# Optimization experiments

Hardware: AMD Instinct MI355X
Metric: run time of the kernel (lower is better)

## Reference

```python
import jax, jax.numpy as jnp
import numpy as np

E = 262144   # num edges
T = 1048576  # num triplets
H = 128      # hidden_channels
IE = 64      # int_emb_size
NR = 6       # num_radial
NS = 7       # num_spherical
BD = 8       # basis_emb_size_dist
BA = 8       # basis_emb_size_angle


def setup_inputs() -> dict:
    key = jax.random.key(0)
    ks = jax.random.split(key, 32)
    def rnd(k, shape, s=0.1):
        return jax.random.normal(k, shape, dtype=jnp.float32) * s
    return {
        "x1": rnd(ks[0], (T, H), 1.0),
        "x_old": rnd(ks[1], (E, H), 1.0),
        "rbf0": rnd(ks[2], (E, NR), 1.0),
        "sbf": rnd(ks[3], (T, NS * NR), 1.0),
        "idx_kj": jax.random.randint(ks[4], (T,), 0, E),
        "idx_ji": jax.random.randint(ks[5], (T,), 0, E),
        "W_rbf1": rnd(ks[6], (NR, BD)),
        "W_rbf2": rnd(ks[7], (BD, H)),
        "W_sbf1": rnd(ks[8], (NS * NR, BA)),
        "W_sbf2": rnd(ks[9], (BA, IE)),
        "W_rbf": rnd(ks[10], (NR, H)),
        "W_kj": rnd(ks[11], (H, H)), "b_kj": rnd(ks[12], (H,)),
        "W_ji": rnd(ks[13], (H, H)), "b_ji": rnd(ks[14], (H,)),
        "W_connect": rnd(ks[15], (H, H)), "b_connect": rnd(ks[16], (H,)),
        "W_get_up": rnd(ks[17], (H, H)), "b_get_up": rnd(ks[18], (H,)),
        "W_down": rnd(ks[19], (H, IE)), "b_down": rnd(ks[20], (IE,)),
        "W_up": rnd(ks[21], (IE, H)), "b_up": rnd(ks[22], (H,)),
        "res_before_W": rnd(ks[23], (1, 2, H, H)), "res_before_b": rnd(ks[24], (1, 2, H)),
        "W_lin": rnd(ks[25], (H, H)), "b_lin": rnd(ks[26], (H,)),
        "res_after_W": rnd(ks[27], (2, 2, H, H)), "res_after_b": rnd(ks[28], (2, 2, H)),
    }


def _residual(x, W, b):
    # x + act(lin2(act(lin1(x))))
    h = jax.nn.silu(x @ W[0] + b[0])
    return x + jax.nn.silu(h @ W[1] + b[1])


def reference(x1, x_old, rbf0, sbf, idx_kj, idx_ji, W_rbf1, W_rbf2, W_sbf1, W_sbf2,
              W_rbf, W_kj, b_kj, W_ji, b_ji, W_connect, b_connect, W_get_up, b_get_up,
              W_down, b_down, W_up, b_up, res_before_W, res_before_b, W_lin, b_lin,
              res_after_W, res_after_b):
    act = jax.nn.silu  # swish
    nE = x_old.shape[0]
    # aggregate plane features onto edges
    x_up = jax.ops.segment_sum(x1, idx_ji, num_segments=nE)
    x_up = act(x_up @ W_get_up + b_get_up)
    x_ji = act(x_old @ W_ji + b_ji)
    x_kj = act(x_old @ W_kj + b_kj)
    rbf = (rbf0 @ W_rbf1) @ W_rbf2            # [E, H]
    x_kj = x_kj * rbf
    x_kj = act(x_kj @ W_down + b_down)        # [E, IE]
    sbf_p = (sbf @ W_sbf1) @ W_sbf2           # [T, IE]
    x_kj = x_kj[idx_kj] * sbf_p               # gather edges -> triplets
    x_kj = jax.ops.segment_sum(x_kj, idx_ji, num_segments=nE)  # scatter back to edges
    x_kj = act(x_kj @ W_up + b_up)
    e1 = x_ji + x_kj
    e1 = act(e1 @ W_connect + b_connect) + x_up
    for i in range(res_before_W.shape[0]):
        e1 = _residual(e1, res_before_W[i], res_before_b[i])
    e1 = act(e1 @ W_lin + b_lin) + x_old
    for i in range(res_after_W.shape[0]):
        e1 = _residual(e1, res_after_W[i], res_after_b[i])
    e2 = (rbf0 @ W_rbf) * e1
    return (e1, e2)
```

## Files before the change

### kernel.cpp

```cpp
#include <hip/hip_runtime.h>

#define E_N 262144
#define T_N 1048576

typedef short  bf16x8  __attribute__((ext_vector_type(8)));
typedef float  f32x4   __attribute__((ext_vector_type(4)));

#define OFF_KJ    0
#define OFF_DOWN  16384
#define OFF_UP    24576
#define OFF_JI    32768
#define OFF_GU    49152
#define OFF_CN    65536
#define OFF_RB0   81920
#define OFF_RB1   98304
#define OFF_LIN   114688
#define OFF_RA00  131072
#define OFF_RA01  147456
#define OFF_RA10  163840
#define OFF_RA11  180224
#define OFF_END   196608
#define WREG_BYTES 524288u

#define OFFB_AGG   0u
#define OFFB_XKJ   33554432u
#define OFFB_WREG  67108864u
#define OFFB_CNT   67633152u
#define OFFB_POS   68683776u
#define OFFB_TRI   69732352u
#define OFFB_BS    73926656u
#define OFFB_BP    73927680u
#define OFFB_KJP   75497472u
#define OFFB_INV   79691776u

__device__ __forceinline__ float silu_f(float x) {
  float e;
  asm("v_exp_f32_e32 %0, %1" : "=v"(e) : "v"(x * -1.44269504088896f));
  float r;
  asm("v_rcp_f32_e32 %0, %1" : "=v"(r) : "v"(1.0f + e));
  return x * r;
}

__device__ __forceinline__ unsigned short f2bf(float f) {
  union { float f; unsigned int u; } v; v.f = f;
  unsigned int u = v.u;
  return (unsigned short)((u + 0x7fffu + ((u >> 16) & 1u)) >> 16);
}
__device__ __forceinline__ float bf2f(unsigned short h) {
  union { unsigned int u; float f; } v; v.u = ((unsigned int)h) << 16;
  return v.f;
}

__device__ __forceinline__ unsigned cvtpk(float lo, float hi) {
  unsigned r;
  asm("v_cvt_pk_bf16_f32 %0, %1, %2" : "=v"(r) : "v"(lo), "v"(hi));
  return r;
}

__device__ __forceinline__ void lds_barrier() {
  asm volatile("s_waitcnt lgkmcnt(0)" ::: "memory");
  __builtin_amdgcn_s_barrier();
  __builtin_amdgcn_sched_barrier(0);
}

template<int NC, int NR, int NTH>
__device__ __forceinline__ void stage_tile(const float* __restrict__ g, char* __restrict__ lds) {
  constexpr int RB = NC * 2;
  constexpr int C4 = NC / 4;
  for (int i = threadIdx.x; i < NR * C4; i += NTH) {
    int r = i / C4, c4 = i % C4;
    float4 v = *(const float4*)(g + (size_t)r * NC + c4 * 4);
    uint2 u;
    u.x = cvtpk(v.x, v.y);
    u.y = cvtpk(v.z, v.w);
    *(uint2*)(lds + r * RB + ((c4 * 8) ^ ((r & 7) << 4))) = u;
  }
}


template<int MREP, int NREP, int KSTEPS, int RB>
__device__ __forceinline__ void mfma_gemm(const char* __restrict__ lds, int row0, int col0,
                                          const unsigned short* __restrict__ WT, int lane,
                                          f32x4 (&acc)[MREP][NREP]) {
  const int kg = lane >> 4, r15 = lane & 15;
#pragma unroll
  for (int m = 0; m < MREP; ++m)
#pragma unroll
    for (int n = 0; n < NREP; ++n) acc[m][n] = (f32x4){0.f, 0.f, 0.f, 0.f};
  __builtin_amdgcn_s_setprio(1);
#pragma unroll
  for (int kk = 0; kk < KSTEPS; ++kk) {
    bf16x8 a[MREP], bfr[NREP];
#pragma unroll
    for (int m = 0; m < MREP; ++m) {
      int row = row0 + m * 16 + r15;
      a[m] = *(const bf16x8*)(lds + row * RB + ((kk * 64 + kg * 16) ^ ((row & 7) << 4)));
    }
#pragma unroll
    for (int n = 0; n < NREP; ++n) {
      int nt = (col0 >> 4) + n;
      bfr[n] = *(const bf16x8*)(WT + (((nt * KSTEPS + kk) * 4 + kg) << 7) + (r15 << 3));
    }
#pragma unroll
    for (int m = 0; m < MREP; ++m)
#pragma unroll
      for (int n = 0; n < NREP; ++n)
        acc[m][n] = __builtin_amdgcn_mfma_f32_16x16x32_bf16(a[m], bfr[n], acc[m][n], 0, 0, 0);
  }
  __builtin_amdgcn_s_setprio(0);
}

template<int MREP, int NREP, int KSTEPS, int RS>
__device__ __forceinline__ void mfma_gemm_gA(const unsigned short* __restrict__ gA,
                                             int row0, int col0,
                                             const unsigned short* __restrict__ WT, int lane,
                                             f32x4 (&acc)[MREP][NREP]) {
  const int kg = lane >> 4, r15 = lane & 15;
#pragma unroll
  for (int m = 0; m < MREP; ++m)
#pragma unroll
    for (int n = 0; n < NREP; ++n) acc[m][n] = (f32x4){0.f, 0.f, 0.f, 0.f};
  __builtin_amdgcn_s_setprio(1);
#pragma unroll
  for (int kk = 0; kk < KSTEPS; ++kk) {
    bf16x8 a[MREP], bfr[NREP];
#pragma unroll
    for (int m = 0; m < MREP; ++m)
      a[m] = *(const bf16x8*)(gA + (size_t)(row0 + m * 16 + r15) * RS + kk * 32 + kg * 8);
#pragma unroll
    for (int n = 0; n < NREP; ++n) {
      int nt = (col0 >> 4) + n;
      bfr[n] = *(const bf16x8*)(WT + (((nt * KSTEPS + kk) * 4 + kg) << 7) + (r15 << 3));
    }
#pragma unroll
    for (int m = 0; m < MREP; ++m)
#pragma unroll
      for (int n = 0; n < NREP; ++n)
        acc[m][n] = __builtin_amdgcn_mfma_f32_16x16x32_bf16(a[m], bfr[n], acc[m][n], 0, 0, 0);
  }
  __builtin_amdgcn_s_setprio(0);
}

template<int MREP, int NREP, int RB>
__device__ __forceinline__ void write_cd(char* __restrict__ lds, int wrow, int wcol, int lane,
                                         const f32x4 (&v)[MREP][NREP]) {
  const int kg = lane >> 4, r15 = lane & 15;
#pragma unroll
  for (int m = 0; m < MREP; ++m)
#pragma unroll
    for (int n = 0; n < NREP; ++n) {
      int col2 = (wcol + n * 16 + r15) * 2;
      int row0 = wrow + m * 16 + kg * 4;
      unsigned u0 = cvtpk(v[m][n][0], v[m][n][1]);
      unsigned u1 = cvtpk(v[m][n][2], v[m][n][3]);
      *(unsigned short*)(lds + (row0 + 0) * RB + (col2 ^ (((row0 + 0) & 7) << 4))) = (unsigned short)u0;
      *(unsigned short*)(lds + (row0 + 1) * RB + (col2 ^ (((row0 + 1) & 7) << 4))) = (unsigned short)(u0 >> 16);
      *(unsigned short*)(lds + (row0 + 2) * RB + (col2 ^ (((row0 + 2) & 7) << 4))) = (unsigned short)u1;
      *(unsigned short*)(lds + (row0 + 3) * RB + (col2 ^ (((row0 + 3) & 7) << 4))) = (unsigned short)(u1 >> 16);
    }
}

__global__ void __launch_bounds__(256) k_prep(
    const float* __restrict__ W_kj, const float* __restrict__ W_down,
    const float* __restrict__ W_up, const float* __restrict__ W_ji,
    const float* __restrict__ W_get_up, const float* __restrict__ W_connect,
    const float* __restrict__ rbW, const float* __restrict__ W_lin,
    const float* __restrict__ raW,
    const float* __restrict__ W_rbf1, const float* __restrict__ W_rbf2,
    unsigned short* __restrict__ wreg) {
  int b = blockIdx.x;
  if (b == 13) {
    float* W12 = (float*)(wreg + OFF_END);
    for (int i = threadIdx.x; i < 768; i += 256) {
      int r = i >> 7, n = i & 127;
      float s = 0.f;
#pragma unroll
      for (int q = 0; q < 8; ++q) s += W_rbf1[r * 8 + q] * W_rbf2[q * 128 + n];
      W12[i] = s;
    }
    return;
  }
  const float* src; int K = 128, N = 128; int off;
  switch (b) {
    case 0:  src = W_kj;          off = OFF_KJ;  break;
    case 1:  src = W_down;        off = OFF_DOWN; N = 64;  break;
    case 2:  src = W_up;          off = OFF_UP;   K = 64;  break;
    case 3:  src = W_ji;          off = OFF_JI;  break;
    case 4:  src = W_get_up;      off = OFF_GU;  break;
    case 5:  src = W_connect;     off = OFF_CN;  break;
    case 6:  src = rbW;           off = OFF_RB0; break;
    case 7:  src = rbW + 16384;   off = OFF_RB1; break;
    case 8:  src = W_lin;         off = OFF_LIN; break;
    case 9:  src = raW;           off = OFF_RA00; break;
    case 10: src = raW + 16384;   off = OFF_RA01; break;
    case 11: src = raW + 32768;   off = OFF_RA10; break;
    default: src = raW + 49152;   off = OFF_RA11; break;
  }
  unsigned short* dst = wreg + off;
  int KS = K >> 5;
  for (int i = threadIdx.x; i < K * N; i += 256) {
    int k = i / N, n = i % N;
    int kk = k >> 5, kg = (k >> 3) & 3, j = k & 7;
    int nt = n >> 4, r15 = n & 15;
    dst[(((nt * KS + kk) * 4 + kg) << 7) + (r15 << 3) + j] = f2bf(src[i]);
  }
}

__global__ void __launch_bounds__(256) k_hist(const int* __restrict__ idx_ji,
                                              int* __restrict__ counts) {
  int t = blockIdx.x * 256 + threadIdx.x;
  atomicAdd(&counts[idx_ji[t]], 1);
}

__global__ void __launch_bounds__(1024) k_scan1(const int* __restrict__ counts,
                                                int* __restrict__ locpre,
                                                int* __restrict__ bsum) {
  __shared__ int s[1024];
  int i = blockIdx.x * 1024 + threadIdx.x;
  int v = counts[i];
  s[threadIdx.x] = v; __syncthreads();
  for (int o = 1; o < 1024; o <<= 1) {
    int t = (threadIdx.x >= o) ? s[threadIdx.x - o] : 0;
    __syncthreads();
    s[threadIdx.x] += t;
    __syncthreads();
  }
  locpre[i] = s[threadIdx.x] - v;
  if (threadIdx.x == 1023) bsum[blockIdx.x] = s[1023];
}

__global__ void __launch_bounds__(256) k_scan2(const int* __restrict__ bsum,
                                               int* __restrict__ bpre, int* __restrict__ offs) {
  __shared__ int s[256];
  int v = bsum[threadIdx.x];
  s[threadIdx.x] = v; __syncthreads();
  for (int o = 1; o < 256; o <<= 1) {
    int t = (threadIdx.x >= o) ? s[threadIdx.x - o] : 0;
    __syncthreads();
    s[threadIdx.x] += t;
    __syncthreads();
  }
  bpre[threadIdx.x] = s[threadIdx.x] - v;
  if (threadIdx.x == 0) offs[E_N] = T_N;
}

__global__ void __launch_bounds__(1024) k_scan3(const int* __restrict__ locpre,
                                                const int* __restrict__ bpre,
                                                int* __restrict__ offs,
                                                int* __restrict__ pos) {
  int i = blockIdx.x * 1024 + threadIdx.x;
  int v = locpre[i] + bpre[blockIdx.x];
  offs[i] = v;
  pos[i] = v;
}

__global__ void __launch_bounds__(256) k_fill(const int* __restrict__ idx_ji,
                                              const int* __restrict__ idx_kj,
                                              int* __restrict__ pos,
                                              int* __restrict__ tri,
                                              int* __restrict__ inv,
                                              int* __restrict__ kjp) {
  int t = blockIdx.x * 256 + threadIdx.x;
  int e = idx_ji[t];
  int slot = atomicAdd(&pos[e], 1);
  tri[slot] = t;
  inv[t] = slot;
  kjp[slot] = idx_kj[t];
}

__global__ void __launch_bounds__(256) k_sbfp(const float* __restrict__ sbf,
                                              const float* __restrict__ W_sbf1,
                                              const float* __restrict__ W_sbf2,
                                              const int* __restrict__ inv,
                                              unsigned int* __restrict__ sbfp) {
  __shared__ float s_s[336];
  __shared__ float s_t8[8][8];
  int t0 = blockIdx.x * 8;
  const float4* src = (const float4*)(sbf + (size_t)t0 * 42);
  for (int i = threadIdx.x; i < 84; i += 256)
    ((float4*)s_s)[i] = src[i];
  __syncthreads();
  if (threadIdx.x < 64) {
    int w8 = threadIdx.x >> 3, bb = threadIdx.x & 7;
    float s = 0.f;
#pragma unroll
    for (int r = 0; r < 42; ++r) s += s_s[w8 * 42 + r] * W_sbf1[r * 8 + bb];
    s_t8[w8][bb] = s;
  }
  __syncthreads();
  int w8 = threadIdx.x >> 5, jj = threadIdx.x & 31;
  float sp0 = 0.f, sp1 = 0.f;
#pragma unroll
  for (int bb = 0; bb < 8; ++bb) {
    float tv = s_t8[w8][bb];
    sp0 += tv * W_sbf2[bb * 64 + jj * 2];
    sp1 += tv * W_sbf2[bb * 64 + jj * 2 + 1];
  }
  int slot = inv[t0 + w8];
  sbfp[(size_t)slot * 32 + jj] = cvtpk(sp0, sp1);
}

__global__ void __launch_bounds__(256) k_aggB(const int* __restrict__ offs,
                                              const int* __restrict__ kjp,
                                              const unsigned int* __restrict__ sbfp,
                                              const unsigned int* __restrict__ xkj,
                                              unsigned int* __restrict__ agg) {
  int sub = threadIdx.x >> 5, jj = threadIdx.x & 31;
  int e = blockIdx.x * 8 + sub;
  int o0 = offs[e], o1 = offs[e + 1];
  float a0 = 0.f, a1 = 0.f;
  for (int i = o0; i < o1; ++i) {
    int kj = kjp[i];
    unsigned int sv = sbfp[(size_t)i * 32 + jj];
    unsigned int xv = xkj[(size_t)kj * 32 + jj];
    a0 += bf2f((unsigned short)(sv & 0xffff)) * bf2f((unsigned short)(xv & 0xffff));
    a1 += bf2f((unsigned short)(sv >> 16)) * bf2f((unsigned short)(xv >> 16));
  }
  agg[(size_t)e * 32 + jj] = cvtpk(a0, a1);
}

__global__ void __launch_bounds__(256) k_xupg(const int* __restrict__ offs,
                                              const int* __restrict__ tri,
                                              const float* __restrict__ x1,
                                              unsigned int* __restrict__ out) {
  int sub = threadIdx.x >> 6, h2 = threadIdx.x & 63;
  int e = blockIdx.x * 4 + sub;
  int o0 = offs[e], o1 = offs[e + 1];
  float a0 = 0.f, a1 = 0.f;
  for (int i = o0; i < o1; ++i) {
    int t = tri[i];
    float2 v = *(const float2*)(x1 + (size_t)t * 128 + h2 * 2);
    a0 += v.x; a1 += v.y;
  }
  out[(size_t)e * 128 + h2] = cvtpk(a0, a1);
}

__global__ void __launch_bounds__(1024, 4) phaseA(
    const float* __restrict__ x_old, const float* __restrict__ rbf0,
    const unsigned short* __restrict__ wreg,
    const float* __restrict__ b_kj, const float* __restrict__ b_down,
    unsigned short* __restrict__ xkjdown) {
  __shared__ char lds[65536];
  char* B0 = lds;
  char* B1 = lds + 32768;
  const int tid = threadIdx.x, lane = tid & 63, wave = tid >> 6;
  const int kg = lane >> 4, r15 = lane & 15;
  const int wrow = (wave >> 3) * 64;
  const int wcol = (wave & 7) * 16;
  const size_t e_base = (size_t)blockIdx.x * 128;
  const float* W12 = (const float*)(wreg + OFF_END);

  stage_tile<128, 128, 1024>(x_old + e_base * 128, B0);
  lds_barrier();

  f32x4 acc[4][1], val[4][1];
  mfma_gemm<4, 1, 4, 256>(B0, wrow, wcol, wreg + OFF_KJ, lane, acc);
  {
    int col = wcol + r15;
    float bk = b_kj[col];
    float wc[6];
#pragma unroll
    for (int q = 0; q < 6; ++q) wc[q] = W12[q * 128 + col];
#pragma unroll
    for (int m = 0; m < 4; ++m)
#pragma unroll
      for (int r = 0; r < 4; ++r) {
        int row = wrow + m * 16 + kg * 4 + r;
        const float* rp = rbf0 + (e_base + row) * 6;
        float rv = rp[0]*wc[0] + rp[1]*wc[1] + rp[2]*wc[2] + rp[3]*wc[3] + rp[4]*wc[4] + rp[5]*wc[5];
        val[m][0][r] = silu_f(acc[m][0][r] + bk) * rv;
      }
  }
  write_cd<4, 1, 256>(B1, wrow, wcol, lane, val);
  lds_barrier();

  const int wrow2 = (wave >> 1) * 16, wcol2 = (wave & 1) * 32;
  f32x4 a2[1][2];
  mfma_gemm<1, 2, 4, 256>(B1, wrow2, wcol2, wreg + OFF_DOWN, lane, a2);
#pragma unroll
  for (int n = 0; n < 2; ++n) {
    int col = wcol2 + n * 16 + r15;
    float bd = b_down[col];
#pragma unroll
    for (int r = 0; r < 4; ++r) {
      int row = wrow2 + kg * 4 + r;
      xkjdown[(e_base + row) * 64 + col] = f2bf(silu_f(a2[0][n][r] + bd));
    }
  }
}

__global__ void __launch_bounds__(1024, 4) phaseC1(
    const float* __restrict__ x_old, float* __restrict__ e1buf,
    const unsigned short* __restrict__ xup_b,
    const unsigned short* __restrict__ agg, const unsigned short* __restrict__ wreg,
    const float* __restrict__ b_up, const float* __restrict__ b_ji,
    const float* __restrict__ b_get_up, const float* __restrict__ b_connect,
    const float* __restrict__ rbB, const float* __restrict__ b_lin,
    const float* __restrict__ raB,
    const float* __restrict__ rbf0, const float* __restrict__ W_rbf,
    float* __restrict__ e2o) {
  __shared__ char lds[65536];
  char* X0 = lds;
  char* X1 = lds + 32768;
  const int tid = threadIdx.x, lane = tid & 63, wave = tid >> 6;
  const int kg = lane >> 4, r15 = lane & 15;
  const int wrow = (wave >> 3) * 64;
  const int wcol = (wave & 7) * 16;
  const size_t e_base = (size_t)blockIdx.x * 128;

  stage_tile<128, 128, 1024>(x_old + e_base * 128, X1);
  lds_barrier();

  f32x4 acc[4][1], keep[4][1], h[4][1];

  mfma_gemm_gA<4, 1, 2, 64>(agg + e_base * 64, wrow, wcol, wreg + OFF_UP, lane, acc);
#pragma unroll
  for (int m = 0; m < 4; ++m) {
    float bu = b_up[wcol + r15];
#pragma unroll
    for (int r = 0; r < 4; ++r) h[m][0][r] = silu_f(acc[m][0][r] + bu);
  }
  mfma_gemm<4, 1, 4, 256>(X1, wrow, wcol, wreg + OFF_JI, lane, acc);
  {
    float bj = b_ji[wcol + r15];
#pragma unroll
    for (int m = 0; m < 4; ++m)
#pragma unroll
      for (int r = 0; r < 4; ++r) keep[m][0][r] = silu_f(acc[m][0][r] + bj) + h[m][0][r];
  }
  write_cd<4, 1, 256>(X0, wrow, wcol, lane, keep);
  lds_barrier();

  mfma_gemm_gA<4, 1, 4, 256>(xup_b + e_base * 256, wrow, wcol, wreg + OFF_GU, lane, acc);
  {
    float bg = b_get_up[wcol + r15];
#pragma unroll
    for (int m = 0; m < 4; ++m)
#pragma unroll
      for (int r = 0; r < 4; ++r) h[m][0][r] = silu_f(acc[m][0][r] + bg);
  }
  mfma_gemm<4, 1, 4, 256>(X0, wrow, wcol, wreg + OFF_CN, lane, acc);
  {
    float bc = b_connect[wcol + r15];
#pragma unroll
    for (int m = 0; m < 4; ++m)
#pragma unroll
      for (int r = 0; r < 4; ++r) keep[m][0][r] = silu_f(acc[m][0][r] + bc) + h[m][0][r];
  }
  write_cd<4, 1, 256>(X1, wrow, wcol, lane, keep);
  lds_barrier();

  mfma_gemm<4, 1, 4, 256>(X1, wrow, wcol, wreg + OFF_RB0, lane, acc);
  {
    float bv = rbB[wcol + r15];
#pragma unroll
    for (int m = 0; m < 4; ++m)
#pragma unroll
      for (int r = 0; r < 4; ++r) h[m][0][r] = silu_f(acc[m][0][r] + bv);
  }
  write_cd<4, 1, 256>(X0, wrow, wcol, lane, h);
  lds_barrier();

  mfma_gemm<4, 1, 4, 256>(X0, wrow, wcol, wreg + OFF_RB1, lane, acc);
  {
    float bv = rbB[128 + wcol + r15];
#pragma unroll
    for (int m = 0; m < 4; ++m)
#pragma unroll
      for (int r = 0; r < 4; ++r) keep[m][0][r] += silu_f(acc[m][0][r] + bv);
  }
  write_cd<4, 1, 256>(X1, wrow, wcol, lane, keep);
  lds_barrier();

  mfma_gemm<4, 1, 4, 256>(X1, wrow, wcol, wreg + OFF_LIN, lane, acc);
  {
    int col = wcol + r15;
    float bl = b_lin[col];
#pragma unroll
    for (int m = 0; m < 4; ++m)
#pragma unroll
      for (int r = 0; r < 4; ++r) {
        int row = wrow + m * 16 + kg * 4 + r;
        keep[m][0][r] = silu_f(acc[m][0][r] + bl) + x_old[(e_base + row) * 128 + col];
      }
  }
  write_cd<4, 1, 256>(X0, wrow, wcol, lane, keep);
  lds_barrier();

  mfma_gemm<4, 1, 4, 256>(X0, wrow, wcol, wreg + OFF_RA00, lane, acc);
  {
    float bv = raB[wcol + r15];
#pragma unroll
    for (int m = 0; m < 4; ++m)
#pragma unroll
      for (int r = 0; r < 4; ++r) h[m][0][r] = silu_f(acc[m][0][r] + bv);
  }
  write_cd<4, 1, 256>(X1, wrow, wcol, lane, h);
  lds_barrier();

  mfma_gemm<4, 1, 4, 256>(X1, wrow, wcol, wreg + OFF_RA01, lane, acc);
  {
    float bv = raB[128 + wcol + r15];
#pragma unroll
    for (int m = 0; m < 4; ++m)
#pragma unroll
      for (int r = 0; r < 4; ++r) keep[m][0][r] += silu_f(acc[m][0][r] + bv);
  }
  write_cd<4, 1, 256>(X0, wrow, wcol, lane, keep);
  lds_barrier();

  mfma_gemm<4, 1, 4, 256>(X0, wrow, wcol, wreg + OFF_RA10, lane, acc);
  {
    float bv = raB[256 + wcol + r15];
#pragma unroll
    for (int m = 0; m < 4; ++m)
#pragma unroll
      for (int r = 0; r < 4; ++r) h[m][0][r] = silu_f(acc[m][0][r] + bv);
  }
  write_cd<4, 1, 256>(X1, wrow, wcol, lane, h);
  lds_barrier();

  mfma_gemm<4, 1, 4, 256>(X1, wrow, wcol, wreg + OFF_RA11, lane, acc);
  {
    int col = wcol + r15;
    float bv = raB[384 + col];
    float wc[6];
#pragma unroll
    for (int q = 0; q < 6; ++q) wc[q] = W_rbf[q * 128 + col];
#pragma unroll
    for (int m = 0; m < 4; ++m)
#pragma unroll
      for (int r = 0; r < 4; ++r) {
        int row = wrow + m * 16 + kg * 4 + r;
        size_t e = e_base + row;
        float val = keep[m][0][r] + silu_f(acc[m][0][r] + bv);
        e1buf[e * 128 + col] = val;
        if (e2o) {
          const float* rp = rbf0 + e * 6;
          float rv = rp[0]*wc[0] + rp[1]*wc[1] + rp[2]*wc[2] + rp[3]*wc[3] + rp[4]*wc[4] + rp[5]*wc[5];
          e2o[e * 128 + col] = val * rv;
        }
      }
  }
}

__global__ void __launch_bounds__(256) k_e2(const float* __restrict__ e1,
                                            const float* __restrict__ rbf0,
                                            const float* __restrict__ W_rbf,
                                            float* __restrict__ e2) {
  size_t gid = (size_t)blockIdx.x * 256 + threadIdx.x;
  int e = (int)(gid >> 5);
  int c = (int)(gid & 31) << 2;
  float r6[6];
#pragma unroll
  for (int r = 0; r < 6; ++r) r6[r] = rbf0[(size_t)e * 6 + r];
  float4 v = *(const float4*)(e1 + (size_t)e * 128 + c);
  float4 o;
  float rv;
  rv = 0.f;
#pragma unroll
  for (int r = 0; r < 6; ++r) rv += r6[r] * W_rbf[r * 128 + c + 0];
  o.x = v.x * rv;
  rv = 0.f;
#pragma unroll
  for (int r = 0; r < 6; ++r) rv += r6[r] * W_rbf[r * 128 + c + 1];
  o.y = v.y * rv;
  rv = 0.f;
#pragma unroll
  for (int r = 0; r < 6; ++r) rv += r6[r] * W_rbf[r * 128 + c + 2];
  o.z = v.z * rv;
  rv = 0.f;
#pragma unroll
  for (int r = 0; r < 6; ++r) rv += r6[r] * W_rbf[r * 128 + c + 3];
  o.w = v.w * rv;
  *(float4*)(e2 + (size_t)e * 128 + c) = o;
}

extern "C" void kernel_launch(void* const* d_in, const int* in_sizes, int n_in,
                              void* d_out, int out_size, void* d_ws, size_t ws_size,
                              hipStream_t stream) {
  const float* x1        = (const float*)d_in[0];
  const float* x_old     = (const float*)d_in[1];
  const float* rbf0      = (const float*)d_in[2];
  const float* sbf       = (const float*)d_in[3];
  const int*   idx_kj    = (const int*)d_in[4];
  const int*   idx_ji    = (const int*)d_in[5];
  const float* W_rbf1    = (const float*)d_in[6];
  const float* W_rbf2    = (const float*)d_in[7];
  const float* W_sbf1    = (const float*)d_in[8];
  const float* W_sbf2    = (const float*)d_in[9];
  const float* W_rbf     = (const float*)d_in[10];
  const float* W_kj      = (const float*)d_in[11];
  const float* b_kj      = (const float*)d_in[12];
  const float* W_ji      = (const float*)d_in[13];
  const float* b_ji      = (const float*)d_in[14];
  const float* W_connect = (const float*)d_in[15];
  const float* b_connect = (const float*)d_in[16];
  const float* W_get_up  = (const float*)d_in[17];
  const float* b_get_up  = (const float*)d_in[18];
  const float* W_down    = (const float*)d_in[19];
  const float* b_down    = (const float*)d_in[20];
  const float* W_up      = (const float*)d_in[21];
  const float* b_up      = (const float*)d_in[22];
  const float* rbW       = (const float*)d_in[23];
  const float* rbB       = (const float*)d_in[24];
  const float* W_lin     = (const float*)d_in[25];
  const float* b_lin     = (const float*)d_in[26];
  const float* raW       = (const float*)d_in[27];
  const float* raB       = (const float*)d_in[28];

  float* e1buf = (float*)d_out;
  char*  base2 = (char*)d_out + (size_t)E_N * 128 * 4;
  float* e2out = (float*)base2;

  unsigned short* xkj_b = (unsigned short*)(base2 + OFFB_XKJ);
  int* counts = (int*)(base2 + OFFB_CNT);
  int* pos    = (int*)(base2 + OFFB_POS);
  int* tri    = (int*)(base2 + OFFB_TRI);
  int* bsum   = (int*)(base2 + OFFB_BS);
  int* bpre   = (int*)(base2 + OFFB_BP);
  int* kjp    = (int*)(base2 + OFFB_KJP);
  int* inv    = (int*)(base2 + OFFB_INV);

  const size_t need_ws = (size_t)WREG_BYTES + (size_t)E_N * 64 * 2;
  const bool fuse = ws_size >= need_ws;
  unsigned short* wreg  = fuse ? (unsigned short*)d_ws
                               : (unsigned short*)(base2 + OFFB_WREG);
  unsigned short* agg_b = fuse ? (unsigned short*)((char*)d_ws + WREG_BYTES)
                               : (unsigned short*)(base2 + OFFB_AGG);

  unsigned int* sbfp_u = (unsigned int*)e1buf;
  unsigned int* xup_u  = (unsigned int*)e1buf;

  k_prep<<<14, 256, 0, stream>>>(W_kj, W_down, W_up, W_ji, W_get_up, W_connect,
                                 rbW, W_lin, raW, W_rbf1, W_rbf2, wreg);

  hipMemsetAsync(counts, 0, (E_N + 1) * sizeof(int), stream);
  k_hist<<<T_N / 256, 256, 0, stream>>>(idx_ji, counts);
  k_scan1<<<256, 1024, 0, stream>>>(counts, pos, bsum);
  k_scan2<<<1, 256, 0, stream>>>(bsum, bpre, counts);
  k_scan3<<<256, 1024, 0, stream>>>(pos, bpre, counts, pos);
  k_fill<<<T_N / 256, 256, 0, stream>>>(idx_ji, idx_kj, pos, tri, inv, kjp);

  k_sbfp<<<T_N / 8, 256, 0, stream>>>(sbf, W_sbf1, W_sbf2, inv, sbfp_u);

  phaseA<<<E_N / 128, 1024, 0, stream>>>(x_old, rbf0, wreg, b_kj, b_down, xkj_b);

  k_aggB<<<E_N / 8, 256, 0, stream>>>(counts, kjp, sbfp_u,
                                      (const unsigned int*)xkj_b, (unsigned int*)agg_b);

  k_xupg<<<E_N / 4, 256, 0, stream>>>(counts, tri, x1, xup_u);

  phaseC1<<<E_N / 128, 1024, 0, stream>>>(x_old, e1buf, (const unsigned short*)xup_u,
                                          agg_b, wreg,
                                          b_up, b_ji, b_get_up, b_connect, rbB, b_lin, raB,
                                          rbf0, W_rbf, fuse ? e2out : nullptr);
  if (!fuse)
    k_e2<<<E_N * 32 / 256, 256, 0, stream>>>(e1buf, rbf0, W_rbf, e2out);
}
```

Measured before the change: 1.127 ms.

## Transpose MFMA operand roles so each lane owns contiguous output columns

The edge-side GEMM chains now put weights in the MFMA A operand and activations in the B operand. Each lane then holds four consecutive output features of one edge row instead of four rows of one column. LDS write-back becomes one 8-byte store per tile instead of four 2-byte stores. Bias, x_old, e1 and e2 accesses become float4 vector loads and stores, and the rbf0 row is loaded once per lane. The cost is more weight-fragment loads per k-step (four W tiles against one activation tile), and the global output access pattern changes.

```diff
diff --git a/kernel.cpp b/kernel.cpp
--- a/kernel.cpp
+++ b/kernel.cpp
@@ -41,6 +41,13 @@
   return x * r;
 }
 
+__device__ __forceinline__ f32x4 silu4(f32x4 v) {
+  f32x4 r;
+#pragma unroll
+  for (int i = 0; i < 4; ++i) r[i] = silu_f(v[i]);
+  return r;
+}
+
 __device__ __forceinline__ unsigned short f2bf(float f) {
   union { float f; unsigned int u; } v; v.f = f;
   unsigned int u = v.u;
@@ -78,86 +85,66 @@
 }
 
 
-template<int MREP, int NREP, int KSTEPS, int RB>
-__device__ __forceinline__ void mfma_gemm(const char* __restrict__ lds, int row0, int col0,
-                                          const unsigned short* __restrict__ WT, int lane,
-                                          f32x4 (&acc)[MREP][NREP]) {
+template<int MREP, int KSTEPS, int RB>
+__device__ __forceinline__ void mfma_gemm_T(const char* __restrict__ lds, int e0, int nt0,
+                                            const unsigned short* __restrict__ WT, int lane,
+                                            f32x4 (&acc)[MREP]) {
   const int kg = lane >> 4, r15 = lane & 15;
 #pragma unroll
-  for (int m = 0; m < MREP; ++m)
-#pragma unroll
-    for (int n = 0; n < NREP; ++n) acc[m][n] = (f32x4){0.f, 0.f, 0.f, 0.f};
+  for (int m = 0; m < MREP; ++m) acc[m] = (f32x4){0.f, 0.f, 0.f, 0.f};
+  const int row = e0 + r15, sw = (row & 7) << 4;
   __builtin_amdgcn_s_setprio(1);
 #pragma unroll
   for (int kk = 0; kk < KSTEPS; ++kk) {
-    bf16x8 a[MREP], bfr[NREP];
-#pragma unroll
-    for (int m = 0; m < MREP; ++m) {
-      int row = row0 + m * 16 + r15;
-      a[m] = *(const bf16x8*)(lds + row * RB + ((kk * 64 + kg * 16) ^ ((row & 7) << 4)));
-    }
-#pragma unroll
-    for (int n = 0; n < NREP; ++n) {
-      int nt = (col0 >> 4) + n;
-      bfr[n] = *(const bf16x8*)(WT + (((nt * KSTEPS + kk) * 4 + kg) << 7) + (r15 << 3));
-    }
+    bf16x8 xb = *(const bf16x8*)(lds + row * RB + ((kk * 64 + kg * 16) ^ sw));
+    bf16x8 wa[MREP];
 #pragma unroll
     for (int m = 0; m < MREP; ++m)
-#pragma unroll
-      for (int n = 0; n < NREP; ++n)
-        acc[m][n] = __builtin_amdgcn_mfma_f32_16x16x32_bf16(a[m], bfr[n], acc[m][n], 0, 0, 0);
+      wa[m] = *(const bf16x8*)(WT + ((((nt0 + m) * KSTEPS + kk) * 4 + kg) << 7) + (r15 << 3));
+#pragma unroll
+    for (int m = 0; m < MREP; ++m)
+      acc[m] = __builtin_amdgcn_mfma_f32_16x16x32_bf16(wa[m], xb, acc[m], 0, 0, 0);
   }
   __builtin_amdgcn_s_setprio(0);
 }
 
-template<int MREP, int NREP, int KSTEPS, int RS>
-__device__ __forceinline__ void mfma_gemm_gA(const unsigned short* __restrict__ gA,
-                                             int row0, int col0,
-                                             const unsigned short* __restrict__ WT, int lane,
-                                             f32x4 (&acc)[MREP][NREP]) {
+template<int MREP, int KSTEPS, int RS>
+__device__ __forceinline__ void mfma_gemm_T_gB(const unsigned short* __restrict__ gB,
+                                               size_t erow0, int nt0,
+                                               const unsigned short* __restrict__ WT, int lane,
+                                               f32x4 (&acc)[MREP]) {
   const int kg = lane >> 4, r15 = lane & 15;
 #pragma unroll
-  for (int m = 0; m < MREP; ++m)
-#pragma unroll
-    for (int n = 0; n < NREP; ++n) acc[m][n] = (f32x4){0.f, 0.f, 0.f, 0.f};
+  for (int m = 0; m < MREP; ++m) acc[m] = (f32x4){0.f, 0.f, 0.f, 0.f};
+  const size_t row = erow0 + r15;
   __builtin_amdgcn_s_setprio(1);
 #pragma unroll
   for (int kk = 0; kk < KSTEPS; ++kk) {
-    bf16x8 a[MREP], bfr[NREP];
+    bf16x8 xb = *(const bf16x8*)(gB + row * RS + kk * 32 + kg * 8);
+    bf16x8 wa[MREP];
 #pragma unroll
     for (int m = 0; m < MREP; ++m)
-      a[m] = *(const bf16x8*)(gA + (size_t)(row0 + m * 16 + r15) * RS + kk * 32 + kg * 8);
-#pragma unroll
-    for (int n = 0; n < NREP; ++n) {
-      int nt = (col0 >> 4) + n;
-      bfr[n] = *(const bf16x8*)(WT + (((nt * KSTEPS + kk) * 4 + kg) << 7) + (r15 << 3));
-    }
+      wa[m] = *(const bf16x8*)(WT + ((((nt0 + m) * KSTEPS + kk) * 4 + kg) << 7) + (r15 << 3));
 #pragma unroll
     for (int m = 0; m < MREP; ++m)
-#pragma unroll
-      for (int n = 0; n < NREP; ++n)
-        acc[m][n] = __builtin_amdgcn_mfma_f32_16x16x32_bf16(a[m], bfr[n], acc[m][n], 0, 0, 0);
+      acc[m] = __builtin_amdgcn_mfma_f32_16x16x32_bf16(wa[m], xb, acc[m], 0, 0, 0);
   }
   __builtin_amdgcn_s_setprio(0);
 }
 
-template<int MREP, int NREP, int RB>
-__device__ __forceinline__ void write_cd(char* __restrict__ lds, int wrow, int wcol, int lane,
-                                         const f32x4 (&v)[MREP][NREP]) {
+template<int MREP, int RB>
+__device__ __forceinline__ void write_cd_T(char* __restrict__ lds, int e0, int nbase, int lane,
+                                           const f32x4 (&v)[MREP]) {
   const int kg = lane >> 4, r15 = lane & 15;
-#pragma unroll
-  for (int m = 0; m < MREP; ++m)
-#pragma unroll
-    for (int n = 0; n < NREP; ++n) {
-      int col2 = (wcol + n * 16 + r15) * 2;
-      int row0 = wrow + m * 16 + kg * 4;
-      unsigned u0 = cvtpk(v[m][n][0], v[m][n][1]);
-      unsigned u1 = cvtpk(v[m][n][2], v[m][n][3]);
-      *(unsigned short*)(lds + (row0 + 0) * RB + (col2 ^ (((row0 + 0) & 7) << 4))) = (unsigned short)u0;
-      *(unsigned short*)(lds + (row0 + 1) * RB + (col2 ^ (((row0 + 1) & 7) << 4))) = (unsigned short)(u0 >> 16);
-      *(unsigned short*)(lds + (row0 + 2) * RB + (col2 ^ (((row0 + 2) & 7) << 4))) = (unsigned short)u1;
-      *(unsigned short*)(lds + (row0 + 3) * RB + (col2 ^ (((row0 + 3) & 7) << 4))) = (unsigned short)(u1 >> 16);
-    }
+  const int row = e0 + r15, sw = (row & 7) << 4;
+#pragma unroll
+  for (int m = 0; m < MREP; ++m) {
+    int off = (nbase + m * 16 + kg * 4) * 2;
+    uint2 u;
+    u.x = cvtpk(v[m][0], v[m][1]);
+    u.y = cvtpk(v[m][2], v[m][3]);
+    *(uint2*)(lds + row * RB + (off ^ sw)) = u;
+  }
 }
 
 __global__ void __launch_bounds__(256) k_prep(
@@ -345,47 +332,53 @@
   char* B1 = lds + 32768;
   const int tid = threadIdx.x, lane = tid & 63, wave = tid >> 6;
   const int kg = lane >> 4, r15 = lane & 15;
-  const int wrow = (wave >> 3) * 64;
-  const int wcol = (wave & 7) * 16;
+  const int e0 = (wave & 7) * 16;
+  const int ngrp = wave >> 3;
+  const int nbase = ngrp * 64, ntb = ngrp * 4;
   const size_t e_base = (size_t)blockIdx.x * 128;
+  const size_t e_lane = e_base + e0 + r15;
   const float* W12 = (const float*)(wreg + OFF_END);
 
   stage_tile<128, 128, 1024>(x_old + e_base * 128, B0);
   lds_barrier();
 
-  f32x4 acc[4][1], val[4][1];
-  mfma_gemm<4, 1, 4, 256>(B0, wrow, wcol, wreg + OFF_KJ, lane, acc);
+  f32x4 acc[4], val[4];
+  mfma_gemm_T<4, 4, 256>(B0, e0, ntb, wreg + OFF_KJ, lane, acc);
   {
-    int col = wcol + r15;
-    float bk = b_kj[col];
-    float wc[6];
-#pragma unroll
-    for (int q = 0; q < 6; ++q) wc[q] = W12[q * 128 + col];
-#pragma unroll
-    for (int m = 0; m < 4; ++m)
-#pragma unroll
-      for (int r = 0; r < 4; ++r) {
-        int row = wrow + m * 16 + kg * 4 + r;
-        const float* rp = rbf0 + (e_base + row) * 6;
-        float rv = rp[0]*wc[0] + rp[1]*wc[1] + rp[2]*wc[2] + rp[3]*wc[3] + rp[4]*wc[4] + rp[5]*wc[5];
-        val[m][0][r] = silu_f(acc[m][0][r] + bk) * rv;
+    float rp[6];
+#pragma unroll
+    for (int q = 0; q < 6; ++q) rp[q] = rbf0[e_lane * 6 + q];
+#pragma unroll
+    for (int m = 0; m < 4; ++m) {
+      int n0 = nbase + m * 16 + kg * 4;
+      f32x4 bk = *(const f32x4*)(b_kj + n0);
+      f32x4 rv = (f32x4){0.f, 0.f, 0.f, 0.f};
+#pragma unroll
+      for (int q = 0; q < 6; ++q) {
+        f32x4 w = *(const f32x4*)(W12 + q * 128 + n0);
+#pragma unroll
+        for (int r = 0; r < 4; ++r) rv[r] += rp[q] * w[r];
       }
-  }
-  write_cd<4, 1, 256>(B1, wrow, wcol, lane, val);
-  lds_barrier();
-
-  const int wrow2 = (wave >> 1) * 16, wcol2 = (wave & 1) * 32;
-  f32x4 a2[1][2];
-  mfma_gemm<1, 2, 4, 256>(B1, wrow2, wcol2, wreg + OFF_DOWN, lane, a2);
-#pragma unroll
-  for (int n = 0; n < 2; ++n) {
-    int col = wcol2 + n * 16 + r15;
-    float bd = b_down[col];
-#pragma unroll
-    for (int r = 0; r < 4; ++r) {
-      int row = wrow2 + kg * 4 + r;
-      xkjdown[(e_base + row) * 64 + col] = f2bf(silu_f(a2[0][n][r] + bd));
+      f32x4 s = silu4(acc[m] + bk);
+#pragma unroll
+      for (int r = 0; r < 4; ++r) val[m][r] = s[r] * rv[r];
     }
+  }
+  write_cd_T<4, 256>(B1, e0, nbase, lane, val);
+  lds_barrier();
+
+  const int nb2 = (wave >> 3) * 32, nt2 = (wave >> 3) * 2;
+  f32x4 a2[2];
+  mfma_gemm_T<2, 4, 256>(B1, e0, nt2, wreg + OFF_DOWN, lane, a2);
+#pragma unroll
+  for (int m = 0; m < 2; ++m) {
+    int n0 = nb2 + m * 16 + kg * 4;
+    f32x4 bd = *(const f32x4*)(b_down + n0);
+    f32x4 s = silu4(a2[m] + bd);
+    uint2 u;
+    u.x = cvtpk(s[0], s[1]);
+    u.y = cvtpk(s[2], s[3]);
+    *(uint2*)(xkjdown + e_lane * 64 + n0) = u;
   }
 }
 
@@ -404,143 +397,130 @@
   char* X1 = lds + 32768;
   const int tid = threadIdx.x, lane = tid & 63, wave = tid >> 6;
   const int kg = lane >> 4, r15 = lane & 15;
-  const int wrow = (wave >> 3) * 64;
-  const int wcol = (wave & 7) * 16;
+  const int e0 = (wave & 7) * 16;
+  const int ngrp = wave >> 3;
+  const int nbase = ngrp * 64, ntb = ngrp * 4;
   const size_t e_base = (size_t)blockIdx.x * 128;
+  const size_t e_lane = e_base + e0 + r15;
 
   stage_tile<128, 128, 1024>(x_old + e_base * 128, X1);
   lds_barrier();
 
-  f32x4 acc[4][1], keep[4][1], h[4][1];
-
-  mfma_gemm_gA<4, 1, 2, 64>(agg + e_base * 64, wrow, wcol, wreg + OFF_UP, lane, acc);
-#pragma unroll
-  for (int m = 0; m < 4; ++m) {
-    float bu = b_up[wcol + r15];
-#pragma unroll
-    for (int r = 0; r < 4; ++r) h[m][0][r] = silu_f(acc[m][0][r] + bu);
-  }
-  mfma_gemm<4, 1, 4, 256>(X1, wrow, wcol, wreg + OFF_JI, lane, acc);
+  f32x4 acc[4], keep[4], h[4];
+
+  mfma_gemm_T_gB<4, 2, 64>(agg, e_base + e0, ntb, wreg + OFF_UP, lane, acc);
+#pragma unroll
+  for (int m = 0; m < 4; ++m) {
+    f32x4 b = *(const f32x4*)(b_up + nbase + m * 16 + kg * 4);
+    h[m] = silu4(acc[m] + b);
+  }
+  mfma_gemm_T<4, 4, 256>(X1, e0, ntb, wreg + OFF_JI, lane, acc);
+#pragma unroll
+  for (int m = 0; m < 4; ++m) {
+    f32x4 b = *(const f32x4*)(b_ji + nbase + m * 16 + kg * 4);
+    keep[m] = silu4(acc[m] + b) + h[m];
+  }
+  write_cd_T<4, 256>(X0, e0, nbase, lane, keep);
+  lds_barrier();
+
+  mfma_gemm_T_gB<4, 4, 256>(xup_b, e_base + e0, ntb, wreg + OFF_GU, lane, acc);
+#pragma unroll
+  for (int m = 0; m < 4; ++m) {
+    f32x4 b = *(const f32x4*)(b_get_up + nbase + m * 16 + kg * 4);
+    h[m] = silu4(acc[m] + b);
+  }
+  mfma_gemm_T<4, 4, 256>(X0, e0, ntb, wreg + OFF_CN, lane, acc);
+#pragma unroll
+  for (int m = 0; m < 4; ++m) {
+    f32x4 b = *(const f32x4*)(b_connect + nbase + m * 16 + kg * 4);
+    keep[m] = silu4(acc[m] + b) + h[m];
+  }
+  write_cd_T<4, 256>(X1, e0, nbase, lane, keep);
+  lds_barrier();
+
+  mfma_gemm_T<4, 4, 256>(X1, e0, ntb, wreg + OFF_RB0, lane, acc);
+#pragma unroll
+  for (int m = 0; m < 4; ++m) {
+    f32x4 b = *(const f32x4*)(rbB + nbase + m * 16 + kg * 4);
+    h[m] = silu4(acc[m] + b);
+  }
+  write_cd_T<4, 256>(X0, e0, nbase, lane, h);
+  lds_barrier();
+
+  mfma_gemm_T<4, 4, 256>(X0, e0, ntb, wreg + OFF_RB1, lane, acc);
+#pragma unroll
+  for (int m = 0; m < 4; ++m) {
+    f32x4 b = *(const f32x4*)(rbB + 128 + nbase + m * 16 + kg * 4);
+    keep[m] += silu4(acc[m] + b);
+  }
+  write_cd_T<4, 256>(X1, e0, nbase, lane, keep);
+  lds_barrier();
+
+  mfma_gemm_T<4, 4, 256>(X1, e0, ntb, wreg + OFF_LIN, lane, acc);
+#pragma unroll
+  for (int m = 0; m < 4; ++m) {
+    int n0 = nbase + m * 16 + kg * 4;
+    f32x4 b = *(const f32x4*)(b_lin + n0);
+    f32x4 xo = *(const f32x4*)(x_old + e_lane * 128 + n0);
+    keep[m] = silu4(acc[m] + b) + xo;
+  }
+  write_cd_T<4, 256>(X0, e0, nbase, lane, keep);
+  lds_barrier();
+
+  mfma_gemm_T<4, 4, 256>(X0, e0, ntb, wreg + OFF_RA00, lane, acc);
+#pragma unroll
+  for (int m = 0; m < 4; ++m) {
+    f32x4 b = *(const f32x4*)(raB + nbase + m * 16 + kg * 4);
+    h[m] = silu4(acc[m] + b);
+  }
+  write_cd_T<4, 256>(X1, e0, nbase, lane, h);
+  lds_barrier();
+
+  mfma_gemm_T<4, 4, 256>(X1, e0, ntb, wreg + OFF_RA01, lane, acc);
+#pragma unroll
+  for (int m = 0; m < 4; ++m) {
+    f32x4 b = *(const f32x4*)(raB + 128 + nbase + m * 16 + kg * 4);
+    keep[m] += silu4(acc[m] + b);
+  }
+  write_cd_T<4, 256>(X0, e0, nbase, lane, keep);
+  lds_barrier();
+
+  mfma_gemm_T<4, 4, 256>(X0, e0, ntb, wreg + OFF_RA10, lane, acc);
+#pragma unroll
+  for (int m = 0; m < 4; ++m) {
+    f32x4 b = *(const f32x4*)(raB + 256 + nbase + m * 16 + kg * 4);
+    h[m] = silu4(acc[m] + b);
+  }
+  write_cd_T<4, 256>(X1, e0, nbase, lane, h);
+  lds_barrier();
+
+  mfma_gemm_T<4, 4, 256>(X1, e0, ntb, wreg + OFF_RA11, lane, acc);
   {
-    float bj = b_ji[wcol + r15];
-#pragma unroll
-    for (int m = 0; m < 4; ++m)
-#pragma unroll
-      for (int r = 0; r < 4; ++r) keep[m][0][r] = silu_f(acc[m][0][r] + bj) + h[m][0][r];
-  }
-  write_cd<4, 1, 256>(X0, wrow, wcol, lane, keep);
-  lds_barrier();
-
-  mfma_gemm_gA<4, 1, 4, 256>(xup_b + e_base * 256, wrow, wcol, wreg + OFF_GU, lane, acc);
-  {
-    float bg = b_get_up[wcol + r15];
-#pragma unroll
-    for (int m = 0; m < 4; ++m)
-#pragma unroll
-      for (int r = 0; r < 4; ++r) h[m][0][r] = silu_f(acc[m][0][r] + bg);
-  }
-  mfma_gemm<4, 1, 4, 256>(X0, wrow, wcol, wreg + OFF_CN, lane, acc);
-  {
-    float bc = b_connect[wcol + r15];
-#pragma unroll
-    for (int m = 0; m < 4; ++m)
-#pragma unroll
-      for (int r = 0; r < 4; ++r) keep[m][0][r] = silu_f(acc[m][0][r] + bc) + h[m][0][r];
-  }
-  write_cd<4, 1, 256>(X1, wrow, wcol, lane, keep);
-  lds_barrier();
-
-  mfma_gemm<4, 1, 4, 256>(X1, wrow, wcol, wreg + OFF_RB0, lane, acc);
-  {
-    float bv = rbB[wcol + r15];
-#pragma unroll
-    for (int m = 0; m < 4; ++m)
-#pragma unroll
-      for (int r = 0; r < 4; ++r) h[m][0][r] = silu_f(acc[m][0][r] + bv);
-  }
-  write_cd<4, 1, 256>(X0, wrow, wcol, lane, h);
-  lds_barrier();
-
-  mfma_gemm<4, 1, 4, 256>(X0, wrow, wcol, wreg + OFF_RB1, lane, acc);
-  {
-    float bv = rbB[128 + wcol + r15];
-#pragma unroll
-    for (int m = 0; m < 4; ++m)
-#pragma unroll
-      for (int r = 0; r < 4; ++r) keep[m][0][r] += silu_f(acc[m][0][r] + bv);
-  }
-  write_cd<4, 1, 256>(X1, wrow, wcol, lane, keep);
-  lds_barrier();
-
-  mfma_gemm<4, 1, 4, 256>(X1, wrow, wcol, wreg + OFF_LIN, lane, acc);
-  {
-    int col = wcol + r15;
-    float bl = b_lin[col];
-#pragma unroll
-    for (int m = 0; m < 4; ++m)
-#pragma unroll
-      for (int r = 0; r < 4; ++r) {
-        int row = wrow + m * 16 + kg * 4 + r;
-        keep[m][0][r] = silu_f(acc[m][0][r] + bl) + x_old[(e_base + row) * 128 + col];
+    float rp[6];
+    if (e2o) {
+#pragma unroll
+      for (int q = 0; q < 6; ++q) rp[q] = rbf0[e_lane * 6 + q];
+    }
+#pragma unroll
+    for (int m = 0; m < 4; ++m) {
+      int n0 = nbase + m * 16 + kg * 4;
+      f32x4 b = *(const f32x4*)(raB + 384 + n0);
+      f32x4 val = keep[m] + silu4(acc[m] + b);
+      *(f32x4*)(e1buf + e_lane * 128 + n0) = val;
+      if (e2o) {
+        f32x4 rv = (f32x4){0.f, 0.f, 0.f, 0.f};
+#pragma unroll
+        for (int q = 0; q < 6; ++q) {
+          f32x4 w = *(const f32x4*)(W_rbf + q * 128 + n0);
+#pragma unroll
+          for (int r = 0; r < 4; ++r) rv[r] += rp[q] * w[r];
+        }
+        f32x4 o;
+#pragma unroll
+        for (int r = 0; r < 4; ++r) o[r] = val[r] * rv[r];
+        *(f32x4*)(e2o + e_lane * 128 + n0) = o;
       }
-  }
-  write_cd<4, 1, 256>(X0, wrow, wcol, lane, keep);
-  lds_barrier();
-
-  mfma_gemm<4, 1, 4, 256>(X0, wrow, wcol, wreg + OFF_RA00, lane, acc);
-  {
-    float bv = raB[wcol + r15];
-#pragma unroll
-    for (int m = 0; m < 4; ++m)
-#pragma unroll
-      for (int r = 0; r < 4; ++r) h[m][0][r] = silu_f(acc[m][0][r] + bv);
-  }
-  write_cd<4, 1, 256>(X1, wrow, wcol, lane, h);
-  lds_barrier();
-
-  mfma_gemm<4, 1, 4, 256>(X1, wrow, wcol, wreg + OFF_RA01, lane, acc);
-  {
-    float bv = raB[128 + wcol + r15];
-#pragma unroll
-    for (int m = 0; m < 4; ++m)
-#pragma unroll
-      for (int r = 0; r < 4; ++r) keep[m][0][r] += silu_f(acc[m][0][r] + bv);
-  }
-  write_cd<4, 1, 256>(X0, wrow, wcol, lane, keep);
-  lds_barrier();
-
-  mfma_gemm<4, 1, 4, 256>(X0, wrow, wcol, wreg + OFF_RA10, lane, acc);
-  {
-    float bv = raB[256 + wcol + r15];
-#pragma unroll
-    for (int m = 0; m < 4; ++m)
-#pragma unroll
-      for (int r = 0; r < 4; ++r) h[m][0][r] = silu_f(acc[m][0][r] + bv);
-  }
-  write_cd<4, 1, 256>(X1, wrow, wcol, lane, h);
-  lds_barrier();
-
-  mfma_gemm<4, 1, 4, 256>(X1, wrow, wcol, wreg + OFF_RA11, lane, acc);
-  {
-    int col = wcol + r15;
-    float bv = raB[384 + col];
-    float wc[6];
-#pragma unroll
-    for (int q = 0; q < 6; ++q) wc[q] = W_rbf[q * 128 + col];
-#pragma unroll
-    for (int m = 0; m < 4; ++m)
-#pragma unroll
-      for (int r = 0; r < 4; ++r) {
-        int row = wrow + m * 16 + kg * 4 + r;
-        size_t e = e_base + row;
-        float val = keep[m][0][r] + silu_f(acc[m][0][r] + bv);
-        e1buf[e * 128 + col] = val;
-        if (e2o) {
-          const float* rp = rbf0 + e * 6;
-          float rv = rp[0]*wc[0] + rp[1]*wc[1] + rp[2]*wc[2] + rp[3]*wc[3] + rp[4]*wc[4] + rp[5]*wc[5];
-          e2o[e * 128 + col] = val * rv;
-        }
-      }
+    }
   }
 }
 
```

After: 1.189 ms. 5.5% more time.
